# Performance work log

Measured on AMD Instinct MI355X. Metric: run time of the kernel, lower is better.

The kernel has to match this reference:

```python
import jax, jax.numpy as jnp
import numpy as np
from jax import lax

WINDOW = 11
C1 = (0.01 * 1) ** 2
C2 = (0.03 * 1) ** 2


def setup_inputs() -> dict:
    key = jax.random.key(0)
    kx, ky = jax.random.split(key)
    x = jax.random.uniform(kx, (8, 3, 512, 512), dtype=jnp.float32)
    y = jax.random.uniform(ky, (8, 3, 512, 512), dtype=jnp.float32)
    return {"x": x, "y": y}


def _window_sum(a):
    # sum over every overlapping WINDOW x WINDOW patch (stride 1, valid)
    return lax.reduce_window(a, 0.0, lax.add,
                             (1, 1, WINDOW, WINDOW),
                             (1, 1, 1, 1), 'VALID')


def reference(x, y):
    # x, y: [B, C, H, W] images in [0, 1]
    n = float(WINDOW * WINDOW)
    sx = _window_sum(x)
    sy = _window_sum(y)
    sxx = _window_sum(x * x)
    syy = _window_sum(y * y)
    sxy = _window_sum(x * y)
    mx = sx / n
    my = sy / n
    # unbiased variance / covariance (matches torch var(unbiased=True) and
    # the bessel-corrected covariance in the original)
    vx = (sxx - n * mx * mx) / (n - 1.0)
    vy = (syy - n * my * my) / (n - 1.0)
    cov = (sxy - n * mx * my) / (n - 1.0)
    ssim = (2.0 * mx * my + C1) * (2.0 * cov + C2) / (
        (mx * mx + my * my + C1) * (vx + vy + C2))
    # original averages over windows (dim 0) and channels (dim 2) -> per-batch
    return (1.0 - ssim.mean(axis=(1, 2, 3))) / 2.0
```

## Files before the change

kernel.cpp:

```cpp
#include <hip/hip_runtime.h>

#define WINDOW 11
#define H 512
#define W 512
#define OH 502
#define OW 502
#define NCH 3
#define BATCH 8
#define RSTRIPE 32
#define NSTRIPES 16
#define NGRP 5
#define GRPW 118
#define WAVES_PER_IMG (NSTRIPES * NGRP)
#define NWAVES (BATCH * NCH * WAVES_PER_IMG)
#define WAVES_PER_BATCH (NCH * WAVES_PER_IMG)
#define NXCD 8
#define CHUNK (NWAVES / NXCD)

#define NPIX_PER_BATCH (3.0f * 502.0f * 502.0f)

template <int CTRL, int RM>
__device__ __forceinline__ float scan_step(float x) {
    int s = __builtin_amdgcn_update_dpp(0, __builtin_bit_cast(int, x),
                                        CTRL, RM, 0xf, false);
    return x + __builtin_bit_cast(float, s);
}
__device__ __forceinline__ float wave_iscan(float x) {
    x = scan_step<0x111, 0xf>(x);
    x = scan_step<0x112, 0xf>(x);
    x = scan_step<0x114, 0xf>(x);
    x = scan_step<0x118, 0xf>(x);
    x = scan_step<0x142, 0xa>(x);
    x = scan_step<0x143, 0xc>(x);
    return x;
}

__device__ __forceinline__ float ssim_from(float sx, float sy, float s2, float sxy) {
    const float n = 121.0f;
    const float inv_n = 1.0f / 121.0f;
    const float inv_nm1 = 1.0f / 120.0f;
    const float c1 = 1e-4f;
    const float c2 = 9e-4f;
    float mx  = sx * inv_n;
    float my  = sy * inv_n;
    float mxy = mx * my;
    float m2  = mx * mx + my * my;
    float cov = (sxy - n * mxy) * inv_nm1;
    float v2  = (s2  - n * m2)  * inv_nm1;
    float num = (2.f * mxy + c1) * (2.f * cov + c2);
    float den = (m2 + c1) * (v2 + c2);
    return num * __builtin_amdgcn_rcpf(den);
}

__global__ __launch_bounds__(64) void ssim_main(const float* __restrict__ x,
                                                const float* __restrict__ y,
                                                float* __restrict__ partials) {
    const int lane = threadIdx.x & 63;

    const int wg    = blockIdx.x;
    const int w_lin = (wg % NXCD) * CHUNK + wg / NXCD;

    const int img = w_lin / WAVES_PER_IMG;
    const int rem = w_lin % WAVES_PER_IMG;
    const int grp = rem / NSTRIPES;
    const int rs  = rem % NSTRIPES;

    const int i0 = rs * RSTRIPE;
    const int i1 = min(i0 + RSTRIPE, OH);
    const int cstart = grp * GRPW;
    const int outw   = min(GRPW, OW - cstart);
    const int c0 = min(cstart + 2 * lane, W - 2);
    const bool tapActive = (2 * lane < outw);

    const float* __restrict__ xi = x + (size_t)img * H * W;
    const float* __restrict__ yi = y + (size_t)img * H * W;
    const float* xc = xi + c0;
    const float* yc = yi + c0;

    float4 v0 = make_float4(0.f, 0.f, 0.f, 0.f);
    float4 v1 = make_float4(0.f, 0.f, 0.f, 0.f);
#pragma unroll
    for (int r = 0; r < WINDOW; ++r) {
        float2 a = *(const float2*)(xc + (size_t)(i0 + r) * W);
        float2 b = *(const float2*)(yc + (size_t)(i0 + r) * W);
        v0.x += a.x; v0.y += b.x; v0.z += a.x * a.x + b.x * b.x; v0.w += a.x * b.x;
        v1.x += a.y; v1.y += b.y; v1.z += a.y * a.y + b.y * b.y; v1.w += a.y * b.y;
    }

#define LD(j, xo, yo, xn, yn) do {                                  \
        int jc_ = min((j), H - 1);                                   \
        int rn_ = min((j) + WINDOW, H - 1);                          \
        xo = *(const float2*)(xc + (size_t)jc_ * W);                 \
        yo = *(const float2*)(yc + (size_t)jc_ * W);                 \
        xn = *(const float2*)(xc + (size_t)rn_ * W);                 \
        yn = *(const float2*)(yc + (size_t)rn_ * W);                 \
    } while (0)

#define SLIDE(xo, yo, xn, yn) do {                                   \
        v0.x += xn.x - xo.x;                                          \
        v0.y += yn.x - yo.x;                                          \
        v0.z += xn.x * xn.x + yn.x * yn.x - xo.x * xo.x - yo.x * yo.x;\
        v0.w += xn.x * yn.x - xo.x * yo.x;                            \
        v1.x += xn.y - xo.y;                                          \
        v1.y += yn.y - yo.y;                                          \
        v1.z += xn.y * xn.y + yn.y * yn.y - xo.y * xo.y - yo.y * yo.y;\
        v1.w += xn.y * yn.y - xo.y * yo.y;                            \
    } while (0)

    float acc = 0.f;

#define COMPUTE() do {                                                        \
        float Tx = v0.x + v1.x, Ty = v0.y + v1.y;                             \
        float Tz = v0.z + v1.z, Tw = v0.w + v1.w;                             \
        float Sx = wave_iscan(Tx), Sy = wave_iscan(Ty);                       \
        float Sz = wave_iscan(Tz), Sw = wave_iscan(Tw);                       \
        int src = lane + 5;                                                   \
        float Ax = __shfl(Sx, src, 64), Ay = __shfl(Sy, src, 64);             \
        float Az = __shfl(Sz, src, 64), Aw = __shfl(Sw, src, 64);             \
        float Bx = __shfl(v1.x, src, 64), By = __shfl(v1.y, src, 64);         \
        float Bz = __shfl(v1.z, src, 64), Bw = __shfl(v1.w, src, 64);         \
        if (tapActive) {                                                      \
            acc += ssim_from(Ax - Bx - Sx + Tx, Ay - By - Sy + Ty,            \
                             Az - Bz - Sz + Tz, Aw - Bw - Sw + Tw);           \
            acc += ssim_from(Ax - Sx + v1.x, Ay - Sy + v1.y,                  \
                             Az - Sz + v1.z, Aw - Sw + v1.w);                 \
        }                                                                     \
    } while (0)

    float2 xoA, yoA, xnA, ynA, xoB, yoB, xnB, ynB;
    LD(i0,     xoA, yoA, xnA, ynA);
    LD(i0 + 1, xoB, yoB, xnB, ynB);
    for (int i = i0; i < i1; i += 2) {
        COMPUTE();
        SLIDE(xoA, yoA, xnA, ynA);
        LD(i + 2, xoA, yoA, xnA, ynA);
        COMPUTE();
        SLIDE(xoB, yoB, xnB, ynB);
        LD(i + 3, xoB, yoB, xnB, ynB);
    }

    for (int off = 32; off > 0; off >>= 1)
        acc += __shfl_down(acc, off, 64);
    if (lane == 0) partials[w_lin] = acc;
}

__global__ __launch_bounds__(256) void ssim_reduce(const float* __restrict__ partials,
                                                   float* __restrict__ out) {
    const int b = blockIdx.x;
    const int t = threadIdx.x;
    float s = 0.f;
    for (int k = t; k < WAVES_PER_BATCH; k += 256)
        s += partials[b * WAVES_PER_BATCH + k];
    for (int off = 32; off > 0; off >>= 1)
        s += __shfl_down(s, off, 64);
    __shared__ float red[4];
    int wid = t >> 6, lane = t & 63;
    if (lane == 0) red[wid] = s;
    __syncthreads();
    if (t == 0) {
        float tot = (red[0] + red[1]) + (red[2] + red[3]);
        out[b] = (1.0f - tot / NPIX_PER_BATCH) * 0.5f;
    }
}

extern "C" void kernel_launch(void* const* d_in, const int* in_sizes, int n_in,
                              void* d_out, int out_size, void* d_ws, size_t ws_size,
                              hipStream_t stream) {
    const float* x = (const float*)d_in[0];
    const float* y = (const float*)d_in[1];
    float* out      = (float*)d_out;
    float* partials = (float*)d_ws;

    ssim_main<<<NWAVES, 64, 0, stream>>>(x, y, partials);
    ssim_reduce<<<BATCH, 256, 0, stream>>>(partials, out);
}
```

Before: 27.45 us.

## Widen lanes to four columns and fuse final reduction via atomic last-wave election

New measurement: 82.57 us. 3.01x slower.

```diff
diff --git a/kernel.cpp b/kernel.cpp
--- a/kernel.cpp
+++ b/kernel.cpp
@@ -9,13 +9,13 @@
 #define BATCH 8
 #define RSTRIPE 32
 #define NSTRIPES 16
-#define NGRP 5
-#define GRPW 118
+#define NGRP 3
 #define WAVES_PER_IMG (NSTRIPES * NGRP)
 #define NWAVES (BATCH * NCH * WAVES_PER_IMG)
 #define WAVES_PER_BATCH (NCH * WAVES_PER_IMG)
 #define NXCD 8
 #define CHUNK (NWAVES / NXCD)
+#define CNT_OFFSET 8192
 
 #define NPIX_PER_BATCH (3.0f * 502.0f * 502.0f)
 
@@ -33,6 +33,17 @@
     x = scan_step<0x142, 0xa>(x);
     x = scan_step<0x143, 0xc>(x);
     return x;
+}
+
+__device__ __forceinline__ float4 f4add(float4 a, float4 b) {
+    return make_float4(a.x + b.x, a.y + b.y, a.z + b.z, a.w + b.w);
+}
+__device__ __forceinline__ float4 f4sub(float4 a, float4 b) {
+    return make_float4(a.x - b.x, a.y - b.y, a.z - b.z, a.w - b.w);
+}
+__device__ __forceinline__ float4 shfl4(float4 v, int src) {
+    return make_float4(__shfl(v.x, src, 64), __shfl(v.y, src, 64),
+                       __shfl(v.z, src, 64), __shfl(v.w, src, 64));
 }
 
 __device__ __forceinline__ float ssim_from(float sx, float sy, float s2, float sxy) {
@@ -54,7 +65,9 @@
 
 __global__ __launch_bounds__(64) void ssim_main(const float* __restrict__ x,
                                                 const float* __restrict__ y,
-                                                float* __restrict__ partials) {
+                                                float* __restrict__ partials,
+                                                int* __restrict__ cnt,
+                                                float* __restrict__ out) {
     const int lane = threadIdx.x & 63;
 
     const int wg    = blockIdx.x;
@@ -64,70 +77,83 @@
     const int rem = w_lin % WAVES_PER_IMG;
     const int grp = rem / NSTRIPES;
     const int rs  = rem % NSTRIPES;
+    const int batch = w_lin / WAVES_PER_BATCH;
 
     const int i0 = rs * RSTRIPE;
     const int i1 = min(i0 + RSTRIPE, OH);
-    const int cstart = grp * GRPW;
-    const int outw   = min(GRPW, OW - cstart);
-    const int c0 = min(cstart + 2 * lane, W - 2);
-    const bool tapActive = (2 * lane < outw);
-
-    const float* __restrict__ xi = x + (size_t)img * H * W;
-    const float* __restrict__ yi = y + (size_t)img * H * W;
-    const float* xc = xi + c0;
-    const float* yc = yi + c0;
+    const int base  = (grp == 0) ? 0 : (grp == 1 ? 244 : 256);
+    const int outLo = (grp == 0) ? 0 : (grp == 1 ? 246 : 490);
+    const int outHi = (grp == 0) ? 245 : (grp == 1 ? 489 : 501);
+
+    const int col = base + 4 * lane;
+    const bool m0a = (col     >= outLo) & (col     <= outHi);
+    const bool m1a = (col + 1 >= outLo) & (col + 1 <= outHi);
+    const bool m2a = (col + 2 >= outLo) & (col + 2 <= outHi);
+    const bool m3a = (col + 3 >= outLo) & (col + 3 <= outHi);
+
+    const float* __restrict__ xc = x + (size_t)img * H * W + col;
+    const float* __restrict__ yc = y + (size_t)img * H * W + col;
 
     float4 v0 = make_float4(0.f, 0.f, 0.f, 0.f);
-    float4 v1 = make_float4(0.f, 0.f, 0.f, 0.f);
+    float4 v1 = v0, v2 = v0, v3 = v0;
 #pragma unroll
     for (int r = 0; r < WINDOW; ++r) {
-        float2 a = *(const float2*)(xc + (size_t)(i0 + r) * W);
-        float2 b = *(const float2*)(yc + (size_t)(i0 + r) * W);
+        float4 a = *(const float4*)(xc + (size_t)(i0 + r) * W);
+        float4 b = *(const float4*)(yc + (size_t)(i0 + r) * W);
         v0.x += a.x; v0.y += b.x; v0.z += a.x * a.x + b.x * b.x; v0.w += a.x * b.x;
         v1.x += a.y; v1.y += b.y; v1.z += a.y * a.y + b.y * b.y; v1.w += a.y * b.y;
+        v2.x += a.z; v2.y += b.z; v2.z += a.z * a.z + b.z * b.z; v2.w += a.z * b.z;
+        v3.x += a.w; v3.y += b.w; v3.z += a.w * a.w + b.w * b.w; v3.w += a.w * b.w;
     }
 
 #define LD(j, xo, yo, xn, yn) do {                                  \
         int jc_ = min((j), H - 1);                                   \
         int rn_ = min((j) + WINDOW, H - 1);                          \
-        xo = *(const float2*)(xc + (size_t)jc_ * W);                 \
-        yo = *(const float2*)(yc + (size_t)jc_ * W);                 \
-        xn = *(const float2*)(xc + (size_t)rn_ * W);                 \
-        yn = *(const float2*)(yc + (size_t)rn_ * W);                 \
+        xo = *(const float4*)(xc + (size_t)jc_ * W);                 \
+        yo = *(const float4*)(yc + (size_t)jc_ * W);                 \
+        xn = *(const float4*)(xc + (size_t)rn_ * W);                 \
+        yn = *(const float4*)(yc + (size_t)rn_ * W);                 \
+    } while (0)
+
+#define SL1(v, cN, cO, dN, dO) do {                                  \
+        v.x += cN - cO;                                              \
+        v.y += dN - dO;                                              \
+        v.z += cN * cN + dN * dN - cO * cO - dO * dO;                \
+        v.w += cN * dN - cO * dO;                                    \
     } while (0)
 
 #define SLIDE(xo, yo, xn, yn) do {                                   \
-        v0.x += xn.x - xo.x;                                          \
-        v0.y += yn.x - yo.x;                                          \
-        v0.z += xn.x * xn.x + yn.x * yn.x - xo.x * xo.x - yo.x * yo.x;\
-        v0.w += xn.x * yn.x - xo.x * yo.x;                            \
-        v1.x += xn.y - xo.y;                                          \
-        v1.y += yn.y - yo.y;                                          \
-        v1.z += xn.y * xn.y + yn.y * yn.y - xo.y * xo.y - yo.y * yo.y;\
-        v1.w += xn.y * yn.y - xo.y * yo.y;                            \
+        SL1(v0, xn.x, xo.x, yn.x, yo.x);                             \
+        SL1(v1, xn.y, xo.y, yn.y, yo.y);                             \
+        SL1(v2, xn.z, xo.z, yn.z, yo.z);                             \
+        SL1(v3, xn.w, xo.w, yn.w, yo.w);                             \
     } while (0)
 
     float acc = 0.f;
 
 #define COMPUTE() do {                                                        \
-        float Tx = v0.x + v1.x, Ty = v0.y + v1.y;                             \
-        float Tz = v0.z + v1.z, Tw = v0.w + v1.w;                             \
-        float Sx = wave_iscan(Tx), Sy = wave_iscan(Ty);                       \
-        float Sz = wave_iscan(Tz), Sw = wave_iscan(Tw);                       \
-        int src = lane + 5;                                                   \
-        float Ax = __shfl(Sx, src, 64), Ay = __shfl(Sy, src, 64);             \
-        float Az = __shfl(Sz, src, 64), Aw = __shfl(Sw, src, 64);             \
-        float Bx = __shfl(v1.x, src, 64), By = __shfl(v1.y, src, 64);         \
-        float Bz = __shfl(v1.z, src, 64), Bw = __shfl(v1.w, src, 64);         \
-        if (tapActive) {                                                      \
-            acc += ssim_from(Ax - Bx - Sx + Tx, Ay - By - Sy + Ty,            \
-                             Az - Bz - Sz + Tz, Aw - Bw - Sw + Tw);           \
-            acc += ssim_from(Ax - Sx + v1.x, Ay - Sy + v1.y,                  \
-                             Az - Sz + v1.z, Aw - Sw + v1.w);                 \
-        }                                                                     \
-    } while (0)
-
-    float2 xoA, yoA, xnA, ynA, xoB, yoB, xnB, ynB;
+        float4 T = f4add(f4add(v0, v1), f4add(v2, v3));                       \
+        float4 S = make_float4(wave_iscan(T.x), wave_iscan(T.y),              \
+                               wave_iscan(T.z), wave_iscan(T.w));             \
+        float4 L    = f4sub(S, T);                                            \
+        float4 p0   = f4add(L, v0);                                           \
+        float4 p01  = f4add(p0, v1);                                          \
+        float4 p012 = f4add(p01, v2);                                         \
+        float4 A012 = shfl4(p012, lane + 2);                                  \
+        float4 AS   = shfl4(S,    lane + 2);                                  \
+        float4 B0   = shfl4(p0,   lane + 3);                                  \
+        float4 B01  = shfl4(p01,  lane + 3);                                  \
+        float4 W0 = f4sub(A012, L);                                           \
+        float4 W1 = f4sub(AS,   p0);                                          \
+        float4 W2 = f4sub(B0,   p01);                                         \
+        float4 W3 = f4sub(B01,  p012);                                        \
+        acc += m0a ? ssim_from(W0.x, W0.y, W0.z, W0.w) : 0.f;                 \
+        acc += m1a ? ssim_from(W1.x, W1.y, W1.z, W1.w) : 0.f;                 \
+        acc += m2a ? ssim_from(W2.x, W2.y, W2.z, W2.w) : 0.f;                 \
+        acc += m3a ? ssim_from(W3.x, W3.y, W3.z, W3.w) : 0.f;                 \
+    } while (0)
+
+    float4 xoA, yoA, xnA, ynA, xoB, yoB, xnB, ynB;
     LD(i0,     xoA, yoA, xnA, ynA);
     LD(i0 + 1, xoB, yoB, xnB, ynB);
     for (int i = i0; i < i1; i += 2) {
@@ -141,25 +167,25 @@
 
     for (int off = 32; off > 0; off >>= 1)
         acc += __shfl_down(acc, off, 64);
-    if (lane == 0) partials[w_lin] = acc;
-}
-
-__global__ __launch_bounds__(256) void ssim_reduce(const float* __restrict__ partials,
-                                                   float* __restrict__ out) {
-    const int b = blockIdx.x;
-    const int t = threadIdx.x;
-    float s = 0.f;
-    for (int k = t; k < WAVES_PER_BATCH; k += 256)
-        s += partials[b * WAVES_PER_BATCH + k];
-    for (int off = 32; off > 0; off >>= 1)
-        s += __shfl_down(s, off, 64);
-    __shared__ float red[4];
-    int wid = t >> 6, lane = t & 63;
-    if (lane == 0) red[wid] = s;
-    __syncthreads();
-    if (t == 0) {
-        float tot = (red[0] + red[1]) + (red[2] + red[3]);
-        out[b] = (1.0f - tot / NPIX_PER_BATCH) * 0.5f;
+
+    int elected = 0;
+    if (lane == 0) {
+        partials[w_lin] = acc;
+        __threadfence();
+        int old = __hip_atomic_fetch_add(&cnt[batch], 1, __ATOMIC_ACQ_REL,
+                                         __HIP_MEMORY_SCOPE_AGENT);
+        elected = (old == WAVES_PER_BATCH - 1);
+    }
+    elected = __shfl(elected, 0, 64);
+    if (elected) {
+        __threadfence();
+        const float* pb = partials + batch * WAVES_PER_BATCH;
+        float s = pb[lane] + pb[lane + 64];
+        if (lane < WAVES_PER_BATCH - 128) s += pb[lane + 128];
+        for (int off = 32; off > 0; off >>= 1)
+            s += __shfl_down(s, off, 64);
+        if (lane == 0)
+            out[batch] = (1.0f - s / NPIX_PER_BATCH) * 0.5f;
     }
 }
 
@@ -170,7 +196,8 @@
     const float* y = (const float*)d_in[1];
     float* out      = (float*)d_out;
     float* partials = (float*)d_ws;
-
-    ssim_main<<<NWAVES, 64, 0, stream>>>(x, y, partials);
-    ssim_reduce<<<BATCH, 256, 0, stream>>>(partials, out);
-}
+    int*   cnt      = (int*)((char*)d_ws + CNT_OFFSET);
+
+    hipMemsetAsync(cnt, 0, BATCH * sizeof(int), stream);
+    ssim_main<<<NWAVES, 64, 0, stream>>>(x, y, partials, cnt, out);
+}
```
